# Kernel tuning notes

Measured on AMD Instinct MI355X. Metric: run time of the kernel, lower is better.

Reference implementation:

```python
import jax, jax.numpy as jnp
import numpy as np

B, C, H, W = 4, 512, 64, 64


def setup_inputs() -> dict:
    key = jax.random.key(0)
    k1, k2, k3, k4, k5 = jax.random.split(key, 5)
    s = 0.02
    return {
        "x": jax.random.normal(k1, (B, C, H, W), dtype=jnp.float32),
        "qkv_w": jax.random.normal(k2, (3 * C, C), dtype=jnp.float32) * s,
        "qkv_b": jax.random.normal(k3, (3 * C,), dtype=jnp.float32) * s,
        "proj_w": jax.random.normal(k4, (C, C), dtype=jnp.float32) * s,
        "proj_b": jax.random.normal(k5, (C,), dtype=jnp.float32) * s,
    }


def reference(x, qkv_w, qkv_b, proj_w, proj_b):
    # NOTE: the original module creates a GroupNorm but never calls it in
    # forward(), so x feeds the 1x1 qkv conv directly.
    b, c, h, w_ = x.shape
    n = h * w_
    xf = x.reshape(b, c, n)  # [B, C, N]
    # 1x1 conv == channel matmul
    qkv = jnp.einsum('oc,bcn->bon', qkv_w, xf) + qkv_b[None, :, None]  # [B, 3C, N]
    q, k, v = qkv[:, :c], qkv[:, c:2 * c], qkv[:, 2 * c:]
    scale = jnp.float32(c) ** -0.5
    # scores[b, i, j] = q_i . k_j  (i, j over spatial positions)
    scores = jnp.einsum('bci,bcj->bij', q, k) * scale  # [B, N, N]
    attn = jax.nn.softmax(scores, axis=2)
    # out_i = sum_j attn[i, j] * v_j
    hmat = jnp.einsum('bij,bcj->bci', attn, v)  # [B, C, N]
    out = jnp.einsum('oc,bcn->bon', proj_w, hmat) + proj_b[None, :, None]
    return x + out.reshape(b, c, h, w_)
```

## Files before the change

### kernel.cpp

```cpp
#include <hip/hip_runtime.h>


using u16 = unsigned short;
using u32 = unsigned int;
using h8   = __attribute__((ext_vector_type(8)))  short;
using fx4  = __attribute__((ext_vector_type(4)))  float;
using f16x = __attribute__((ext_vector_type(16))) float;
using q16  = __attribute__((ext_vector_type(4)))  u32;
using u16x4= __attribute__((ext_vector_type(4)))  u16;

#define BB 4
#define CC 512
#define NN 4096
#define NBE ((size_t)BB * NN * CC)

#define GLOBAL_AS __attribute__((address_space(1)))
#define LDS_AS    __attribute__((address_space(3)))
#define GLOAD_LDS(src, dst) \
  __builtin_amdgcn_global_load_lds((const GLOBAL_AS u32*)(const void*)(src), \
                                   (LDS_AS u32*)(void*)(dst), 16, 0, 0)

__device__ __forceinline__ u16 f2b(float f) {
  u32 u = __float_as_uint(f);
  u = (u + 0x7fffu + ((u >> 16) & 1u)) >> 16;
  return (u16)u;
}
__device__ __forceinline__ float b2f(u16 h) { return __uint_as_float(((u32)h) << 16); }

__global__ void k_prep(const float* __restrict__ qw, const float* __restrict__ pw,
                       u16* __restrict__ wqb, u16* __restrict__ wpb) {
  int i = blockIdx.x * 256 + threadIdx.x;
  if (i < 1536 * 512) wqb[i] = f2b(qw[i]);
  if (i < 512 * 512)  wpb[i] = f2b(pw[i]);
}

__global__ __launch_bounds__(256) void k_txp(const float* __restrict__ x, u16* __restrict__ xt) {
  int bid = blockIdx.x;
  int nb = bid & 63; int cb = (bid >> 6) & 7; int b = bid >> 9;
  __shared__ float t[64][65];
  const float* xb = x + (size_t)b * CC * NN;
  for (int k = 0; k < 16; ++k) {
    int idx = k * 256 + threadIdx.x;
    int r = idx >> 6, col = idx & 63;
    t[r][col] = xb[(size_t)(cb * 64 + r) * NN + nb * 64 + col];
  }
  __syncthreads();
  u16* xtb = xt + (size_t)b * NN * CC;
  for (int k = 0; k < 16; ++k) {
    int idx = k * 256 + threadIdx.x;
    int nr = idx >> 6, cc = idx & 63;
    xtb[(size_t)(nb * 64 + nr) * CC + cb * 64 + cc] = f2b(t[cc][nr]);
  }
}

__device__ __forceinline__ void gemm_mm(const char* __restrict__ Ab, const char* __restrict__ Bb,
                                        q16* aT, q16* bT, fx4 (&acc)[4][4], int tid) {
  const int lane = tid & 63, wv = tid >> 6;
  const int wm = wv >> 1, wn = wv & 1, g = lane >> 4, r = lane & 15;
  for (int kb = 0; kb < 8; ++kb) {
    __syncthreads();
#pragma unroll
    for (int it = 0; it < 4; ++it) {
      int idx = it * 256 + tid; int row = idx >> 3, slot = idx & 7;
      size_t go = (size_t)row * 1024 + (size_t)kb * 128 + (size_t)slot * 16;
      aT[row * 8 + (slot ^ (row & 7))] = *(const q16*)(Ab + go);
      bT[row * 8 + (slot ^ (row & 7))] = *(const q16*)(Bb + go);
    }
    __syncthreads();
#pragma unroll
    for (int ks = 0; ks < 2; ++ks) {
      h8 af[4], bf[4];
#pragma unroll
      for (int mt = 0; mt < 4; ++mt) { int row = wm * 64 + mt * 16 + r; af[mt] = *(const h8*)&aT[row * 8 + ((ks * 4 + g) ^ (row & 7))]; }
#pragma unroll
      for (int nt = 0; nt < 4; ++nt) { int row = wn * 64 + nt * 16 + r; bf[nt] = *(const h8*)&bT[row * 8 + ((ks * 4 + g) ^ (row & 7))]; }
#pragma unroll
      for (int mt = 0; mt < 4; ++mt)
#pragma unroll
        for (int nt = 0; nt < 4; ++nt)
          acc[mt][nt] = __builtin_amdgcn_mfma_f32_16x16x32_bf16(af[mt], bf[nt], acc[mt][nt], 0, 0, 0);
    }
  }
}

__global__ __launch_bounds__(256) void k_qkv(const u16* __restrict__ wqb, const u16* __restrict__ xt,
                                             const float* __restrict__ qkvb,
                                             u16* __restrict__ qt, u16* __restrict__ kt, u16* __restrict__ vv) {
  __shared__ q16 aT[1024], bT[1024];
  int bid = blockIdx.x;
  int nb = bid & 31; int mb = (bid >> 5) % 12; int b = bid / 384;
  int ob = mb * 128, n0 = nb * 128;
  int tid = threadIdx.x, lane = tid & 63, wv = tid >> 6;
  int wm = wv >> 1, wn = wv & 1, g = lane >> 4, r = lane & 15;
  fx4 acc[4][4] = {};
  gemm_mm((const char*)(wqb + (size_t)ob * CC),
          (const char*)(xt + ((size_t)b * NN + n0) * CC), aT, bT, acc, tid);
  int region = mb >> 2;
#pragma unroll
  for (int mt = 0; mt < 4; ++mt) {
    int o_b = ob + wm * 64 + mt * 16 + g * 4;
#pragma unroll
    for (int nt = 0; nt < 4; ++nt) {
      int n = n0 + wn * 64 + nt * 16 + r;
      if (region == 2) {
#pragma unroll
        for (int rr = 0; rr < 4; ++rr) {
          int o = o_b + rr;
          float v = acc[mt][nt][rr] + qkvb[o];
          vv[((size_t)b * CC + (o - 1024)) * NN + n] = f2b(v);
        }
      } else {
        u16x4 pk;
#pragma unroll
        for (int rr = 0; rr < 4; ++rr) {
          int o = o_b + rr;
          float v = acc[mt][nt][rr] + qkvb[o];
          if (region == 0) v *= 0.044194173824159216f;
          pk[rr] = f2b(v);
        }
        u16* dst = (region == 0 ? qt : kt) + ((size_t)b * NN + n) * CC + (o_b - region * 512);
        *(u16x4*)dst = pk;
      }
    }
  }
}

#define BAR_LGKM() do { asm volatile("s_waitcnt lgkmcnt(0)" ::: "memory"); \
  __builtin_amdgcn_sched_barrier(0); __builtin_amdgcn_s_barrier(); \
  __builtin_amdgcn_sched_barrier(0); } while (0)
#define BAR_VM() do { asm volatile("s_waitcnt vmcnt(0) lgkmcnt(0)" ::: "memory"); \
  __builtin_amdgcn_sched_barrier(0); __builtin_amdgcn_s_barrier(); \
  __builtin_amdgcn_sched_barrier(0); } while (0)

__global__ __launch_bounds__(512, 2) void k_attn(const u16* __restrict__ qt, const u16* __restrict__ kt,
                                                 const u16* __restrict__ vv,
                                                 u16* __restrict__ op, float* __restrict__ ml) {
  __shared__ __align__(16) q16 kbuf[2][2048];
  __shared__ __align__(16) q16 vbuf[2][2048];
  __shared__ __align__(16) float sx[8][2][64][4];
  __shared__ __align__(16) u16 pT[128][40];

  int bid = blockIdx.x;
  int bp = bid & 7; int b = bp >> 1, part = bp & 1;
  int qb0 = (bid >> 3) * 128;
  int tid = threadIdx.x, w = tid >> 6, l = tid & 63;
  int ih = w & 3, ch = w >> 2;
  int l31 = l & 31, lh = l >> 5;
  bool lo = (w < 4);

  const u16* ktb = kt + (size_t)b * NN * CC;
  const u16* vvb = vv + (size_t)b * CC * NN;
  int j0 = part * 2048;

  h8 qf[16];
  {
    const u16* qrow = qt + ((size_t)b * NN + qb0 + ih * 32 + l31) * CC + ch * 256 + lh * 8;
#pragma unroll
    for (int ks = 0; ks < 16; ++ks) qf[ks] = *(const h8*)(qrow + ks * 16);
  }

  h8 ones;
#pragma unroll
  for (int e = 0; e < 8; ++e) ones[e] = (short)0x3F80;

  f16x oacc[8] = {};
  f16x lacc = {};

  const u16* ksrc0 = ktb + (size_t)w * CC + (size_t)((l ^ w) * 8);
  const int  vxr   = (l >> 3) & 3;
  const u16* vsrc0 = vvb + (size_t)(w * 16 + (l >> 2)) * NN + ((l & 3) ^ vxr) * 8;

#define STAGE(JB, D) do { \
  _Pragma("unroll") \
  for (int ro = 0; ro < 4; ++ro) { \
    int row = ro * 8 + w; \
    GLOAD_LDS(ksrc0 + ((size_t)(JB) + ro * 8) * CC, &kbuf[D][row * 64]); \
  } \
  _Pragma("unroll") \
  for (int ro = 0; ro < 4; ++ro) { \
    GLOAD_LDS(vsrc0 + (size_t)ro * 128 * NN + (JB), &vbuf[D][ro * 512 + w * 64]); \
  } \
} while (0)

  STAGE(j0, 0);
  BAR_VM();

  int cur = 0;
  const int kxor = l31 & 7;
  const int vrx  = (l31 >> 1) & 3;
  for (int t = 0; t < 64; ++t) {
    if (t < 63) STAGE(j0 + t * 32 + 32, cur ^ 1);

    f16x sacc = {};
#pragma unroll
    for (int ks = 0; ks < 16; ++ks) {
      int o = ch * 32 + ks * 2 + lh;
      h8 kf = *(const h8*)&kbuf[cur][(l31 << 6) + (o ^ kxor)];
      sacc = __builtin_amdgcn_mfma_f32_32x32x16_bf16(qf[ks], kf, sacc, 0, 0, 0);
    }

    {
      fx4 w0, w1;
      if (lo) { w0 = fx4{sacc[8], sacc[9], sacc[10], sacc[11]};
                w1 = fx4{sacc[12], sacc[13], sacc[14], sacc[15]}; }
      else    { w0 = fx4{sacc[0], sacc[1], sacc[2], sacc[3]};
                w1 = fx4{sacc[4], sacc[5], sacc[6], sacc[7]}; }
      *(fx4*)&sx[w][0][l][0] = w0;
      *(fx4*)&sx[w][1][l][0] = w1;
    }
    BAR_LGKM();
    {
      fx4 r0 = *(const fx4*)&sx[w ^ 4][0][l][0];
      fx4 r1 = *(const fx4*)&sx[w ^ 4][1][l][0];
      if (lo) {
#pragma unroll
        for (int q = 0; q < 4; ++q) { sacc[q] += r0[q]; sacc[4 + q] += r1[q]; }
#pragma unroll
        for (int q = 0; q < 8; ++q) {
          float p = __expf(q < 4 ? sacc[q] : sacc[q]);
          int row = ih * 32 + (q & 3) + 8 * (q >> 2) + 4 * lh;
          pT[row][l31] = f2b(p);
        }
      } else {
#pragma unroll
        for (int q = 0; q < 4; ++q) { sacc[8 + q] += r0[q]; sacc[12 + q] += r1[q]; }
#pragma unroll
        for (int q = 0; q < 8; ++q) {
          float p = __expf(sacc[8 + q]);
          int rr = 8 + q;
          int row = ih * 32 + (rr & 3) + 8 * (rr >> 2) + 4 * lh;
          pT[row][l31] = f2b(p);
        }
      }
    }
    BAR_LGKM();

#pragma unroll
    for (int ks = 0; ks < 2; ++ks) {
      h8 pf = *(const h8*)&pT[ih * 32 + l31][ks * 16 + lh * 8];
      lacc = __builtin_amdgcn_mfma_f32_32x32x16_bf16(pf, ones, lacc, 0, 0, 0);
#pragma unroll
      for (int cf = 0; cf < 8; ++cf) {
        int o = ks * 2 + lh;
        int chunk = ch * 1024 + cf * 128 + l31 * 4 + (o ^ vrx);
        h8 vf = *(const h8*)&vbuf[cur][chunk];
        oacc[cf] = __builtin_amdgcn_mfma_f32_32x32x16_bf16(pf, vf, oacc[cf], 0, 0, 0);
      }
    }
    BAR_VM();
    cur ^= 1;
  }

  u16* opb = op + (((size_t)part * BB + b) * NN + qb0) * CC;
#pragma unroll
  for (int cf = 0; cf < 8; ++cf)
#pragma unroll
    for (int rr = 0; rr < 16; ++rr) {
      int row = ih * 32 + (rr & 3) + 8 * (rr >> 2) + 4 * lh;
      int c = ch * 256 + cf * 32 + l31;
      opb[(size_t)row * CC + c] = f2b(oacc[cf][rr]);
    }
  if (l31 == 0 && ch == 0) {
#pragma unroll
    for (int rr = 0; rr < 16; ++rr) {
      int row = ih * 32 + (rr & 3) + 8 * (rr >> 2) + 4 * lh;
      ml[((size_t)part * BB + b) * NN + qb0 + row] = lacc[rr];
    }
  }
}

__global__ __launch_bounds__(256) void k_comb(const u16* __restrict__ op, const float* __restrict__ ml,
                                              u16* __restrict__ ht) {
  int row = blockIdx.x * 4 + (threadIdx.x >> 6);
  int lane = threadIdx.x & 63;
  int b = row >> 12; int i = row & 4095;
  float l1 = ml[((size_t)0 * BB + b) * NN + i];
  float l2 = ml[((size_t)1 * BB + b) * NN + i];
  float inv = 1.0f / (l1 + l2);
  const u16* o1 = op + ((size_t)b * NN + i) * CC + lane * 8;
  const u16* o2 = o1 + NBE;
  h8 a = *(const h8*)o1; h8 c = *(const h8*)o2;
  u16 res[8];
#pragma unroll
  for (int e = 0; e < 8; ++e)
    res[e] = f2b((b2f((u16)a[e]) + b2f((u16)c[e])) * inv);
  *(h8*)(ht + ((size_t)b * NN + i) * CC + lane * 8) = *(const h8*)res;
}

__global__ __launch_bounds__(256) void k_proj(const u16* __restrict__ ht, const u16* __restrict__ wpb,
                                              const float* __restrict__ pb, const float* __restrict__ x,
                                              float* __restrict__ out) {
  __shared__ q16 aT[1024], bT[1024];
  int bid = blockIdx.x;
  int ot = bid & 3; int ntile = (bid >> 2) & 31; int b = bid >> 7;
  int n0 = ntile * 128, o0 = ot * 128;
  int tid = threadIdx.x, lane = tid & 63, wv = tid >> 6;
  int wm = wv >> 1, wn = wv & 1, g = lane >> 4, r = lane & 15;
  fx4 acc[4][4] = {};
  gemm_mm((const char*)(ht + ((size_t)b * NN + n0) * CC),
          (const char*)(wpb + (size_t)o0 * CC), aT, bT, acc, tid);
  const float* xb = x + (size_t)b * CC * NN;
  float* ob_ = out + (size_t)b * CC * NN;
#pragma unroll
  for (int nt = 0; nt < 4; ++nt) {
    int o = o0 + wn * 64 + nt * 16 + r;
    float bias = pb[o];
#pragma unroll
    for (int mt = 0; mt < 4; ++mt) {
      int n = n0 + wm * 64 + mt * 16 + g * 4;
      fx4 xv = *(const fx4*)(xb + (size_t)o * NN + n);
      fx4 res;
#pragma unroll
      for (int rr = 0; rr < 4; ++rr) res[rr] = acc[mt][nt][rr] + bias + xv[rr];
      *(fx4*)(ob_ + (size_t)o * NN + n) = res;
    }
  }
}

extern "C" void kernel_launch(void* const* d_in, const int* in_sizes, int n_in,
                              void* d_out, int out_size, void* d_ws, size_t ws_size,
                              hipStream_t stream) {
  const float* x  = (const float*)d_in[0];
  const float* qw = (const float*)d_in[1];
  const float* qb = (const float*)d_in[2];
  const float* pw = (const float*)d_in[3];
  const float* pb = (const float*)d_in[4];
  float* out = (float*)d_out;

  u16* ws  = (u16*)d_ws;
  u16* qt  = ws;
  u16* kt  = qt + NBE;
  u16* vv  = kt + NBE;
  u16* xt  = vv + NBE;
  u16* ht  = xt + NBE;
  u16* wqb = ht + NBE;
  u16* wpb = wqb + 1536 * 512;
  u16* op  = wpb + 512 * 512;
  float* ml = (float*)(op + 2 * NBE);

  hipLaunchKernelGGL(k_prep, dim3(3072), dim3(256), 0, stream, qw, pw, wqb, wpb);
  hipLaunchKernelGGL(k_txp,  dim3(2048), dim3(256), 0, stream, x, xt);
  hipLaunchKernelGGL(k_qkv,  dim3(1536), dim3(256), 0, stream, wqb, xt, qb, qt, kt, vv);
  hipLaunchKernelGGL(k_attn, dim3(256),  dim3(512), 0, stream, qt, kt, vv, op, ml);
  hipLaunchKernelGGL(k_comb, dim3(4096), dim3(256), 0, stream, op, ml, ht);
  hipLaunchKernelGGL(k_proj, dim3(512),  dim3(256), 0, stream, ht, wpb, pb, x, out);
}
```

Measured before the change: 371.5 us.

## Give each attention wave full channel depth; fuse split combine into projection

The attention kernel is rewritten so each wave owns 16 query rows with all 512 channels, using 16x16x32 MFMAs. This removes the cross-wave partial-score exchange through shared memory and the two block barriers per key tile. The price is 32 output accumulators per wave and one block per CU (launch bounds changed to 1). Separately, the combine kernel is folded into the projection GEMM's A-tile load, which sums the two split partials and normalizes by the row sums, removing one launch and an intermediate buffer round trip.

```diff
diff --git a/kernel.cpp b/kernel.cpp
--- a/kernel.cpp
+++ b/kernel.cpp
@@ -5,7 +5,6 @@
 using u32 = unsigned int;
 using h8   = __attribute__((ext_vector_type(8)))  short;
 using fx4  = __attribute__((ext_vector_type(4)))  float;
-using f16x = __attribute__((ext_vector_type(16))) float;
 using q16  = __attribute__((ext_vector_type(4)))  u32;
 using u16x4= __attribute__((ext_vector_type(4)))  u16;
 
@@ -125,28 +124,22 @@
   }
 }
 
-#define BAR_LGKM() do { asm volatile("s_waitcnt lgkmcnt(0)" ::: "memory"); \
-  __builtin_amdgcn_sched_barrier(0); __builtin_amdgcn_s_barrier(); \
-  __builtin_amdgcn_sched_barrier(0); } while (0)
 #define BAR_VM() do { asm volatile("s_waitcnt vmcnt(0) lgkmcnt(0)" ::: "memory"); \
   __builtin_amdgcn_sched_barrier(0); __builtin_amdgcn_s_barrier(); \
   __builtin_amdgcn_sched_barrier(0); } while (0)
 
-__global__ __launch_bounds__(512, 2) void k_attn(const u16* __restrict__ qt, const u16* __restrict__ kt,
+__global__ __launch_bounds__(512, 1) void k_attn(const u16* __restrict__ qt, const u16* __restrict__ kt,
                                                  const u16* __restrict__ vv,
                                                  u16* __restrict__ op, float* __restrict__ ml) {
   __shared__ __align__(16) q16 kbuf[2][2048];
   __shared__ __align__(16) q16 vbuf[2][2048];
-  __shared__ __align__(16) float sx[8][2][64][4];
-  __shared__ __align__(16) u16 pT[128][40];
+  __shared__ __align__(16) u16 pT[8][16][40];
 
   int bid = blockIdx.x;
   int bp = bid & 7; int b = bp >> 1, part = bp & 1;
   int qb0 = (bid >> 3) * 128;
   int tid = threadIdx.x, w = tid >> 6, l = tid & 63;
-  int ih = w & 3, ch = w >> 2;
-  int l31 = l & 31, lh = l >> 5;
-  bool lo = (w < 4);
+  int g = l >> 4, r = l & 15;
 
   const u16* ktb = kt + (size_t)b * NN * CC;
   const u16* vvb = vv + (size_t)b * CC * NN;
@@ -154,17 +147,17 @@
 
   h8 qf[16];
   {
-    const u16* qrow = qt + ((size_t)b * NN + qb0 + ih * 32 + l31) * CC + ch * 256 + lh * 8;
-#pragma unroll
-    for (int ks = 0; ks < 16; ++ks) qf[ks] = *(const h8*)(qrow + ks * 16);
+    const u16* qrow = qt + ((size_t)b * NN + qb0 + w * 16 + r) * CC + g * 8;
+#pragma unroll
+    for (int ks = 0; ks < 16; ++ks) qf[ks] = *(const h8*)(qrow + ks * 32);
   }
 
   h8 ones;
 #pragma unroll
   for (int e = 0; e < 8; ++e) ones[e] = (short)0x3F80;
 
-  f16x oacc[8] = {};
-  f16x lacc = {};
+  fx4 oacc[32] = {};
+  fx4 lacc = {};
 
   const u16* ksrc0 = ktb + (size_t)w * CC + (size_t)((l ^ w) * 8);
   const int  vxr   = (l >> 3) & 3;
@@ -186,119 +179,110 @@
   BAR_VM();
 
   int cur = 0;
-  const int kxor = l31 & 7;
-  const int vrx  = (l31 >> 1) & 3;
   for (int t = 0; t < 64; ++t) {
     if (t < 63) STAGE(j0 + t * 32 + 32, cur ^ 1);
 
-    f16x sacc = {};
+    fx4 s[2] = {};
 #pragma unroll
     for (int ks = 0; ks < 16; ++ks) {
-      int o = ch * 32 + ks * 2 + lh;
-      h8 kf = *(const h8*)&kbuf[cur][(l31 << 6) + (o ^ kxor)];
-      sacc = __builtin_amdgcn_mfma_f32_32x32x16_bf16(qf[ks], kf, sacc, 0, 0, 0);
-    }
-
-    {
-      fx4 w0, w1;
-      if (lo) { w0 = fx4{sacc[8], sacc[9], sacc[10], sacc[11]};
-                w1 = fx4{sacc[12], sacc[13], sacc[14], sacc[15]}; }
-      else    { w0 = fx4{sacc[0], sacc[1], sacc[2], sacc[3]};
-                w1 = fx4{sacc[4], sacc[5], sacc[6], sacc[7]}; }
-      *(fx4*)&sx[w][0][l][0] = w0;
-      *(fx4*)&sx[w][1][l][0] = w1;
-    }
-    BAR_LGKM();
-    {
-      fx4 r0 = *(const fx4*)&sx[w ^ 4][0][l][0];
-      fx4 r1 = *(const fx4*)&sx[w ^ 4][1][l][0];
-      if (lo) {
-#pragma unroll
-        for (int q = 0; q < 4; ++q) { sacc[q] += r0[q]; sacc[4 + q] += r1[q]; }
-#pragma unroll
-        for (int q = 0; q < 8; ++q) {
-          float p = __expf(q < 4 ? sacc[q] : sacc[q]);
-          int row = ih * 32 + (q & 3) + 8 * (q >> 2) + 4 * lh;
-          pT[row][l31] = f2b(p);
-        }
-      } else {
-#pragma unroll
-        for (int q = 0; q < 4; ++q) { sacc[8 + q] += r0[q]; sacc[12 + q] += r1[q]; }
-#pragma unroll
-        for (int q = 0; q < 8; ++q) {
-          float p = __expf(sacc[8 + q]);
-          int rr = 8 + q;
-          int row = ih * 32 + (rr & 3) + 8 * (rr >> 2) + 4 * lh;
-          pT[row][l31] = f2b(p);
-        }
+#pragma unroll
+      for (int nt = 0; nt < 2; ++nt) {
+        int row = nt * 16 + r;
+        h8 kf = *(const h8*)&kbuf[cur][row * 64 + ((ks * 4 + g) ^ (r & 7))];
+        s[nt] = __builtin_amdgcn_mfma_f32_16x16x32_bf16(qf[ks], kf, s[nt], 0, 0, 0);
       }
     }
-    BAR_LGKM();
-
-#pragma unroll
-    for (int ks = 0; ks < 2; ++ks) {
-      h8 pf = *(const h8*)&pT[ih * 32 + l31][ks * 16 + lh * 8];
-      lacc = __builtin_amdgcn_mfma_f32_32x32x16_bf16(pf, ones, lacc, 0, 0, 0);
-#pragma unroll
-      for (int cf = 0; cf < 8; ++cf) {
-        int o = ks * 2 + lh;
-        int chunk = ch * 1024 + cf * 128 + l31 * 4 + (o ^ vrx);
-        h8 vf = *(const h8*)&vbuf[cur][chunk];
-        oacc[cf] = __builtin_amdgcn_mfma_f32_32x32x16_bf16(pf, vf, oacc[cf], 0, 0, 0);
-      }
-    }
+
+#pragma unroll
+    for (int rr = 0; rr < 4; ++rr) {
+      pT[w][g * 4 + rr][r]      = f2b(__expf(s[0][rr]));
+      pT[w][g * 4 + rr][16 + r] = f2b(__expf(s[1][rr]));
+    }
+    asm volatile("s_waitcnt lgkmcnt(0)" ::: "memory");
+    __builtin_amdgcn_sched_barrier(0);
+
+    h8 pf = *(const h8*)&pT[w][r][g * 8];
+    lacc = __builtin_amdgcn_mfma_f32_16x16x32_bf16(pf, ones, lacc, 0, 0, 0);
+#pragma unroll
+    for (int ct = 0; ct < 32; ++ct) {
+      int c = ct * 16 + r;
+      h8 vf = *(const h8*)&vbuf[cur][c * 4 + (g ^ ((r >> 1) & 3))];
+      oacc[ct] = __builtin_amdgcn_mfma_f32_16x16x32_bf16(pf, vf, oacc[ct], 0, 0, 0);
+    }
+
     BAR_VM();
     cur ^= 1;
   }
 
-  u16* opb = op + (((size_t)part * BB + b) * NN + qb0) * CC;
-#pragma unroll
-  for (int cf = 0; cf < 8; ++cf)
-#pragma unroll
-    for (int rr = 0; rr < 16; ++rr) {
-      int row = ih * 32 + (rr & 3) + 8 * (rr >> 2) + 4 * lh;
-      int c = ch * 256 + cf * 32 + l31;
-      opb[(size_t)row * CC + c] = f2b(oacc[cf][rr]);
-    }
-  if (l31 == 0 && ch == 0) {
-#pragma unroll
-    for (int rr = 0; rr < 16; ++rr) {
-      int row = ih * 32 + (rr & 3) + 8 * (rr >> 2) + 4 * lh;
-      ml[((size_t)part * BB + b) * NN + qb0 + row] = lacc[rr];
-    }
-  }
-}
-
-__global__ __launch_bounds__(256) void k_comb(const u16* __restrict__ op, const float* __restrict__ ml,
-                                              u16* __restrict__ ht) {
-  int row = blockIdx.x * 4 + (threadIdx.x >> 6);
-  int lane = threadIdx.x & 63;
-  int b = row >> 12; int i = row & 4095;
-  float l1 = ml[((size_t)0 * BB + b) * NN + i];
-  float l2 = ml[((size_t)1 * BB + b) * NN + i];
-  float inv = 1.0f / (l1 + l2);
-  const u16* o1 = op + ((size_t)b * NN + i) * CC + lane * 8;
-  const u16* o2 = o1 + NBE;
-  h8 a = *(const h8*)o1; h8 c = *(const h8*)o2;
-  u16 res[8];
-#pragma unroll
-  for (int e = 0; e < 8; ++e)
-    res[e] = f2b((b2f((u16)a[e]) + b2f((u16)c[e])) * inv);
-  *(h8*)(ht + ((size_t)b * NN + i) * CC + lane * 8) = *(const h8*)res;
-}
-
-__global__ __launch_bounds__(256) void k_proj(const u16* __restrict__ ht, const u16* __restrict__ wpb,
+  u16* opb = op + (((size_t)part * BB + b) * NN + qb0 + w * 16) * CC;
+#pragma unroll
+  for (int ct = 0; ct < 32; ++ct)
+#pragma unroll
+    for (int rr = 0; rr < 4; ++rr) {
+      int i = g * 4 + rr; int c = ct * 16 + r;
+      opb[(size_t)i * CC + c] = f2b(oacc[ct][rr]);
+    }
+  if (r == 0) {
+#pragma unroll
+    for (int rr = 0; rr < 4; ++rr)
+      ml[((size_t)part * BB + b) * NN + qb0 + w * 16 + g * 4 + rr] = lacc[rr];
+  }
+}
+
+__global__ __launch_bounds__(256) void k_proj(const u16* __restrict__ op, const float* __restrict__ ml,
+                                              const u16* __restrict__ wpb,
                                               const float* __restrict__ pb, const float* __restrict__ x,
                                               float* __restrict__ out) {
   __shared__ q16 aT[1024], bT[1024];
+  __shared__ float invl[128];
   int bid = blockIdx.x;
   int ot = bid & 3; int ntile = (bid >> 2) & 31; int b = bid >> 7;
   int n0 = ntile * 128, o0 = ot * 128;
   int tid = threadIdx.x, lane = tid & 63, wv = tid >> 6;
   int wm = wv >> 1, wn = wv & 1, g = lane >> 4, r = lane & 15;
+
+  if (tid < 128) {
+    int n = n0 + tid;
+    float l1 = ml[((size_t)0 * BB + b) * NN + n];
+    float l2 = ml[((size_t)1 * BB + b) * NN + n];
+    invl[tid] = 1.0f / (l1 + l2);
+  }
+
+  const char* Ab1 = (const char*)(op + ((size_t)b * NN + n0) * CC);
+  const char* Ab2 = Ab1 + NBE * sizeof(u16);
+  const char* Bb  = (const char*)(wpb + (size_t)o0 * CC);
   fx4 acc[4][4] = {};
-  gemm_mm((const char*)(ht + ((size_t)b * NN + n0) * CC),
-          (const char*)(wpb + (size_t)o0 * CC), aT, bT, acc, tid);
+  for (int kb = 0; kb < 8; ++kb) {
+    __syncthreads();
+#pragma unroll
+    for (int it = 0; it < 4; ++it) {
+      int idx = it * 256 + tid; int row = idx >> 3, slot = idx & 7;
+      size_t go = (size_t)row * 1024 + (size_t)kb * 128 + (size_t)slot * 16;
+      q16 a1 = *(const q16*)(Ab1 + go);
+      q16 a2 = *(const q16*)(Ab2 + go);
+      float iv = invl[row];
+      u16 res[8];
+      const u16* pa1 = (const u16*)&a1; const u16* pa2 = (const u16*)&a2;
+#pragma unroll
+      for (int e = 0; e < 8; ++e) res[e] = f2b((b2f(pa1[e]) + b2f(pa2[e])) * iv);
+      aT[row * 8 + (slot ^ (row & 7))] = *(const q16*)res;
+      bT[row * 8 + (slot ^ (row & 7))] = *(const q16*)(Bb + go);
+    }
+    __syncthreads();
+#pragma unroll
+    for (int ks = 0; ks < 2; ++ks) {
+      h8 af[4], bf[4];
+#pragma unroll
+      for (int mt = 0; mt < 4; ++mt) { int row = wm * 64 + mt * 16 + r; af[mt] = *(const h8*)&aT[row * 8 + ((ks * 4 + g) ^ (row & 7))]; }
+#pragma unroll
+      for (int nt = 0; nt < 4; ++nt) { int row = wn * 64 + nt * 16 + r; bf[nt] = *(const h8*)&bT[row * 8 + ((ks * 4 + g) ^ (row & 7))]; }
+#pragma unroll
+      for (int mt = 0; mt < 4; ++mt)
+#pragma unroll
+        for (int nt = 0; nt < 4; ++nt)
+          acc[mt][nt] = __builtin_amdgcn_mfma_f32_16x16x32_bf16(af[mt], bf[nt], acc[mt][nt], 0, 0, 0);
+    }
+  }
   const float* xb = x + (size_t)b * CC * NN;
   float* ob_ = out + (size_t)b * CC * NN;
 #pragma unroll
@@ -332,8 +316,7 @@
   u16* kt  = qt + NBE;
   u16* vv  = kt + NBE;
   u16* xt  = vv + NBE;
-  u16* ht  = xt + NBE;
-  u16* wqb = ht + NBE;
+  u16* wqb = xt + NBE;
   u16* wpb = wqb + 1536 * 512;
   u16* op  = wpb + 512 * 512;
   float* ml = (float*)(op + 2 * NBE);
@@ -342,6 +325,5 @@
   hipLaunchKernelGGL(k_txp,  dim3(2048), dim3(256), 0, stream, x, xt);
   hipLaunchKernelGGL(k_qkv,  dim3(1536), dim3(256), 0, stream, wqb, xt, qb, qt, kt, vv);
   hipLaunchKernelGGL(k_attn, dim3(256),  dim3(512), 0, stream, qt, kt, vv, op, ml);
-  hipLaunchKernelGGL(k_comb, dim3(4096), dim3(256), 0, stream, op, ml, ht);
-  hipLaunchKernelGGL(k_proj, dim3(512),  dim3(256), 0, stream, ht, wpb, pb, x, out);
-}
+  hipLaunchKernelGGL(k_proj, dim3(512),  dim3(256), 0, stream, op, ml, wpb, pb, x, out);
+}
```

New measurement: 356.3 us. 4.1% less time.
